# Kernel tuning notes

Measured on AMD Instinct MI355X. Metric: run time of the kernel, lower is better.

The kernel has to match this reference:

```python
import jax, jax.numpy as jnp
import numpy as np

B, N, K = 2, 128, 32   # batch, num_agents, irrep embedding dim
KAPPA = 1.0            # kappa_beta temperature
EPS = 1e-8             # cholesky regularization
EPS_SOFT = 1e-8        # softmax stability constant


def setup_inputs() -> dict:
    key = jax.random.key(0)
    k1, k2, k3, k4 = jax.random.split(key, 4)
    mu_q = jax.random.normal(k1, (B, N, K), jnp.float32)
    A = jax.random.normal(k2, (B, N, K, K), jnp.float32)
    # SPD belief covariances: A A^T / K + I
    sigma_q = jnp.einsum('bnkl,bnml->bnkm', A, A) / K + jnp.eye(K, dtype=jnp.float32)
    phi = 0.1 * jax.random.normal(k3, (B, N, 3), jnp.float32)  # small gauge frames
    G = jax.random.normal(k4, (3, K, K), jnp.float32)
    generators = 0.5 * (G - jnp.swapaxes(G, -1, -2))  # antisymmetric so(3) generators
    return {"mu_q": mu_q, "sigma_q": sigma_q, "phi": phi, "generators": generators}


def _expm_batched(X):
    # batched Pade matrix exponential over leading dims
    shp = X.shape
    Y = jax.vmap(jax.scipy.linalg.expm)(X.reshape(-1, shp[-2], shp[-1]))
    return Y.reshape(shp)


def reference(mu_q, sigma_q, phi, generators):
    Bb, Nn, Kk = mu_q.shape
    eye = jnp.eye(Kk, dtype=mu_q.dtype)

    # per-agent gauge frame exponentials: E_n = exp(phi_n . G), Em_n = exp(-phi_n . G)
    X = jnp.einsum('bna,akl->bnkl', phi, generators)
    E = _expm_batched(X)        # (B,N,K,K)
    Em = _expm_batched(-X)      # (B,N,K,K)

    # transported means: Omega_ij mu_j = E_i (Em_j mu_j)
    v = jnp.einsum('bjkl,bjl->bjk', Em, mu_q)              # (B,N,K)
    mu_t = jnp.einsum('bikl,bjl->bijk', E, v)              # (B,N,N,K)

    # transported covariances: Omega_ij Sigma_j Omega_ij^T = E_i (Em_j Sig_j Em_j^T) E_i^T
    S = jnp.einsum('bjkl,bjlm,bjnm->bjkn', Em, sigma_q, Em)          # (B,N,K,K)
    sig_t = jnp.einsum('bikl,bjlm,binm->bijkn', E, S, E)             # (B,N,N,K,K)
    sig_t = 0.5 * (sig_t + jnp.swapaxes(sig_t, -1, -2))              # symmetrize

    # KL(q_i || Omega_ij[q_j]) via Cholesky + triangular solves
    L1 = jnp.linalg.cholesky(sigma_q + EPS * eye)                    # (B,N,K,K)
    L2 = jnp.linalg.cholesky(sig_t + EPS * eye)                      # (B,N,N,K,K)

    # tr(Sig2^{-1} Sig1) = ||L2^{-1} L1||_F^2
    L1b = jnp.broadcast_to(L1[:, :, None], L2.shape)
    Aij = jax.scipy.linalg.solve_triangular(L2, L1b, lower=True)
    trace_term = jnp.sum(Aij * Aij, axis=(-2, -1))                   # (B,N,N)

    # (mu2-mu1)^T Sig2^{-1} (mu2-mu1) = ||L2^{-1} dmu||^2
    dmu = mu_t - mu_q[:, :, None, :]
    y = jax.scipy.linalg.solve_triangular(L2, dmu[..., None], lower=True)[..., 0]
    quad_term = jnp.sum(y * y, axis=-1)                              # (B,N,N)

    logdet1 = 2.0 * jnp.sum(jnp.log(jnp.diagonal(L1, axis1=-2, axis2=-1)), axis=-1)  # (B,N)
    logdet2 = 2.0 * jnp.sum(jnp.log(jnp.diagonal(L2, axis1=-2, axis2=-1)), axis=-1)  # (B,N,N)

    kl = 0.5 * (trace_term + quad_term - Kk + logdet2 - logdet1[:, :, None])
    kl = jnp.maximum(kl, 0.0)

    # attention weights beta_ij = softmax_j(-KL/kappa), then epsilon-renormalize
    beta = jax.nn.softmax(-kl / KAPPA, axis=-1)
    beta = beta + EPS_SOFT
    beta = beta / jnp.sum(beta, axis=-1, keepdims=True)

    # mean-only aggregation: m_i = sum_j beta_ij Omega_ij[mu_j]
    mu_agg = jnp.einsum('bij,bijk->bik', beta, mu_t)
    return mu_agg
```

## Files before the change

kernel.cpp:

```cpp
#include <hip/hip_runtime.h>
#include <math.h>

#define NB 2
#define NA 128
#define KD 32
#define LS 36
#define BN (NB*NA)
#define EPSV 1e-8f

__device__ __align__(16) float g_Q[BN*KD*KD];
__device__ __align__(16) float g_T[BN*KD*KD];
__device__ __align__(16) float g_E[BN*KD*KD];
__device__ __align__(16) float g_v[BN*KD];
__device__ __align__(16) float g_u[BN*KD];
__device__ __align__(16) float g_ld[BN];
__device__ __align__(16) float g_c[BN];

#define O_M   0
#define O_X   1152
#define O_X2  2304
#define O_X4  3456
#define O_B   4608
#define O_W   5760
#define O_E   6912
#define O_F   8064
#define O_VV  9216
#define O_DG  9248
#define O_P   9280
#define O_MU  9792
#define O_LD  9824
#define O_TOT 9828

__device__ __forceinline__ float rdlane(float x, int l) {
  return __int_as_float(__builtin_amdgcn_readlane(__float_as_int(x), l));
}
__device__ __forceinline__ float d4(float4 a, float4 b) {
  return a.x*b.x + a.y*b.y + a.z*b.z + a.w*b.w;
}

__device__ __forceinline__ void mm2(const float* A, const float* B,
                                    int r0, int c0, float acc[2]) {
  #pragma unroll
  for (int q4 = 0; q4 < KD; q4 += 4) {
    const float4 a4 = *(const float4*)&A[r0*LS + q4];
    const float ar[4] = {a4.x, a4.y, a4.z, a4.w};
    #pragma unroll
    for (int u = 0; u < 4; ++u) {
      const float2 b2 = *(const float2*)&B[(q4+u)*LS + c0];
      acc[0] += ar[u]*b2.x; acc[1] += ar[u]*b2.y;
    }
  }
}

__global__ __launch_bounds__(512, 1) void agent_kernel(
    const float* __restrict__ mu_q, const float* __restrict__ sigma_q,
    const float* __restrict__ phi, const float* __restrict__ gen) {
  __shared__ __align__(16) float buf[O_TOT];
  const int g = blockIdx.x;
  const int tid = threadIdx.x;
  const int e0 = tid * 2;
  const int r0 = e0 >> 5;
  const int c0 = e0 & 31;

  const float p0 = phi[g*3+0], p1 = phi[g*3+1], p2 = phi[g*3+2];
  if (tid < KD) buf[O_MU + tid] = mu_q[g*KD + tid];
  {
    const float2 sg = *(const float2*)(sigma_q + (size_t)g*1024 + e0);
    const float2 g0 = *(const float2*)(gen + e0);
    const float2 g1 = *(const float2*)(gen + 1024 + e0);
    const float2 g2 = *(const float2*)(gen + 2048 + e0);
    buf[O_X + r0*LS + c0]     = p0*g0.x + p1*g1.x + p2*g2.x;
    buf[O_X + r0*LS + c0 + 1] = p0*g0.y + p1*g1.y + p2*g2.y;
    buf[O_M + r0*LS + c0]     = sg.x + ((r0 == c0)     ? EPSV : 0.f);
    buf[O_M + r0*LS + c0 + 1] = sg.y + ((r0 == c0 + 1) ? EPSV : 0.f);
  }
  __syncthreads();

  float a2[2] = {0.f, 0.f};
  mm2(buf + O_X, buf + O_X, r0, c0, a2);
  if (c0 == r0)          buf[O_DG + r0] = a2[0];
  else if (c0 + 1 == r0) buf[O_DG + r0] = a2[1];
  __syncthreads();

  float trc = 0.f;
  #pragma unroll
  for (int r = 0; r < KD; ++r) trc += buf[O_DG + r];
  const float anorm = sqrtf(fmaxf(-trc, 0.f));
  int s = 0;
  if (anorm > 1.f) { s = (int)ceilf(log2f(anorm)); s = min(s, 15); }
  const float sc1 = exp2f((float)(-s));
  const float sc2 = sc1 * sc1;
  const float x2v0 = a2[0]*sc2, x2v1 = a2[1]*sc2;
  buf[O_X2 + r0*LS + c0]     = x2v0;
  buf[O_X2 + r0*LS + c0 + 1] = x2v1;
  __syncthreads();

  const float C4 = 1.f/24.f, C5 = 1.f/120.f, C6 = 1.f/720.f, C7 = 1.f/5040.f;
  float a3[2] = {0.f,0.f}, a4[2] = {0.f,0.f};
  mm2(buf + O_X2, buf + O_X,  r0, c0, a3);
  mm2(buf + O_X2, buf + O_X2, r0, c0, a4);
  const float dlt0 = (r0 == c0) ? 1.f : 0.f, dlt1 = (r0 == c0+1) ? 1.f : 0.f;
  const float xs0 = buf[O_X + r0*LS + c0]*sc1, xs1 = buf[O_X + r0*LS + c0+1]*sc1;
  const float x3v0 = a3[0]*sc1, x3v1 = a3[1]*sc1;
  buf[O_X4 + r0*LS + c0]     = a4[0];
  buf[O_X4 + r0*LS + c0 + 1] = a4[1];
  buf[O_B + r0*LS + c0]      = C4*dlt0 + C5*xs0 + C6*x2v0 + C7*x3v0;
  buf[O_B + r0*LS + c0 + 1]  = C4*dlt1 + C5*xs1 + C6*x2v1 + C7*x3v1;
  __syncthreads();

  {
    float u[2] = {0.f, 0.f};
    mm2(buf + O_B, buf + O_X4, r0, c0, u);
    buf[O_E + r0*LS + c0]     = dlt0 + xs0 + 0.5f*x2v0 + (1.f/6.f)*x3v0 + u[0];
    buf[O_E + r0*LS + c0 + 1] = dlt1 + xs1 + 0.5f*x2v1 + (1.f/6.f)*x3v1 + u[1];
  }
  __syncthreads();

  float* pe = buf + O_E;
  float* po = buf + O_F;
  for (int t = 0; t < s; ++t) {
    float ac[2] = {0.f, 0.f};
    mm2(pe, pe, r0, c0, ac);
    po[r0*LS + c0]     = ac[0];
    po[r0*LS + c0 + 1] = ac[1];
    __syncthreads();
    float* tp = pe; pe = po; po = tp;
  }

  if (tid < 64) {
    const int ci = tid & 31;
    float acc[KD];
    #pragma unroll
    for (int r = 0; r < KD; ++r) acc[r] = pe[r*LS + ci];
    float row[KD];
    #pragma unroll
    for (int q4 = 0; q4 < KD; q4 += 4) {
      const float4 m4 = *(const float4*)&buf[O_M + ci*LS + q4];
      row[q4] = m4.x; row[q4+1] = m4.y; row[q4+2] = m4.z; row[q4+3] = m4.w;
    }
    float Lr[KD], dinv[KD];
    float dprod = 1.f;
    #pragma unroll
    for (int j = 0; j < KD; ++j) {
      const float djj = rdlane(row[j], j);
      const float d = sqrtf(djj);
      const float rin = 1.f / d;
      dprod *= d;
      dinv[j] = rin;
      const float lij = row[j] * rin;
      Lr[j] = lij;
      #pragma unroll
      for (int q = j + 1; q < KD; ++q)
        row[q] = fmaf(-lij, rdlane(lij, q), row[q]);
    }
    if (tid == 0) {
      const float ld = 2.f * logf(dprod);
      g_ld[g] = ld;
      buf[O_LD] = ld;
    }
    #pragma unroll
    for (int q = 0; q < KD; ++q) {
      const float wq = acc[q] * dinv[q];
      acc[q] = wq;
      #pragma unroll
      for (int r = q + 1; r < KD; ++r)
        acc[r] = fmaf(-rdlane(Lr[q], r), wq, acc[r]);
    }
    #pragma unroll
    for (int r = 0; r < KD; ++r) buf[O_W + r*LS + ci] = acc[r];
  } else if (tid < 96) {
    const int c = tid - 64;
    float va = 0.f;
    #pragma unroll
    for (int r = 0; r < KD; ++r) va += pe[r*LS + c] * buf[O_MU + r];
    g_v[g*KD + c] = va;
    buf[O_VV + c] = va;
  } else if (tid >= 256) {
    const int t4 = (tid - 256) * 4;
    const int rm = t4 >> 5, cm = t4 & 31;
    float a[4] = {0.f,0.f,0.f,0.f};
    #pragma unroll
    for (int q4 = 0; q4 < KD; q4 += 4) {
      const float4 a4 = *(const float4*)&buf[O_M + rm*LS + q4];
      const float ar[4] = {a4.x, a4.y, a4.z, a4.w};
      #pragma unroll
      for (int u = 0; u < 4; ++u) {
        const float4 b4 = *(const float4*)&pe[(q4+u)*LS + cm];
        a[0] += ar[u]*b4.x; a[1] += ar[u]*b4.y;
        a[2] += ar[u]*b4.z; a[3] += ar[u]*b4.w;
      }
    }
    #pragma unroll
    for (int m = 0; m < 4; ++m) buf[O_B + rm*LS + cm + m] = a[m];
  }
  __syncthreads();

  {
    float aq[2] = {0.f,0.f}, at[2] = {0.f,0.f};
    #pragma unroll
    for (int q = 0; q < KD; ++q) {
      const float wq = buf[O_W + q*LS + r0];
      const float eq = pe[q*LS + r0];
      const float2 wb = *(const float2*)&buf[O_W + q*LS + c0];
      const float2 mb = *(const float2*)&buf[O_B + q*LS + c0];
      aq[0] += wq*wb.x; aq[1] += wq*wb.y;
      at[0] += eq*mb.x; at[1] += eq*mb.y;
    }
    const float vr = buf[O_VV + r0];
    const float vc0 = buf[O_VV + c0], vc1 = buf[O_VV + c0 + 1];
    at[0] += vr * vc0;
    at[1] += vr * vc1;
    *(float2*)&g_Q[(size_t)g*1024 + r0*KD + c0] = make_float2(aq[0], aq[1]);
    *(float2*)&g_T[(size_t)g*1024 + r0*KD + c0] = make_float2(at[0], at[1]);
    *(float2*)&g_E[(size_t)g*1024 + r0*KD + c0] =
        make_float2(pe[r0*LS + c0], pe[r0*LS + c0 + 1]);
    buf[O_P + r0*16 + (c0 >> 1)] = aq[0]*vc0 + aq[1]*vc1;
  }
  __syncthreads();

  if (tid < KD) {
    float u = 0.f;
    #pragma unroll
    for (int m = 0; m < 16; ++m) u += buf[O_P + tid*16 + m];
    g_u[g*KD + tid] = u;
    float t = u * buf[O_VV + tid];
    #pragma unroll
    for (int o = 1; o < 32; o <<= 1) t += __shfl_xor(t, o);
    if (tid == 0) g_c[g] = 0.5f*(t + buf[O_LD] - (float)KD);
  }
}

__global__ __launch_bounds__(512, 1) void pair_kernel(float* __restrict__ out) {
  const int g = blockIdx.x;
  const int b = g >> 7;
  const int i = g & (NA - 1);
  const int tid = threadIdx.x;
  __shared__ __align__(16) float sv[NA*KD];
  __shared__ __align__(16) float su[NA*KD];
  __shared__ float sc[NA];
  __shared__ float skl[NA];
  __shared__ float sbe[NA];
  __shared__ float sp[16*KD];
  __shared__ float sw[KD];

  {
    const float4* vs = (const float4*)(g_v + (size_t)b*NA*KD);
    const float4* us = (const float4*)(g_u + (size_t)b*NA*KD);
    float4* dv = (float4*)sv;
    float4* du = (float4*)su;
    dv[tid]       = vs[tid];
    dv[tid + 512] = vs[tid + 512];
    du[tid]       = us[tid];
    du[tid + 512] = us[tid + 512];
    if (tid < NA) sc[tid] = g_c[b*NA + tid];
  }

  const int lane = tid & 63;
  const int wave = tid >> 6;
  const int k  = lane >> 1;
  const int l0 = (lane & 1) * 16;
  const bool even = (lane & 1) == 0;

  float4 t0, t1, t2, t3;
  {
    const float4* Tp = (const float4*)(g_T + (size_t)g*1024 + k*KD + l0);
    t0 = Tp[0]; t1 = Tp[1]; t2 = Tp[2]; t3 = Tp[3];
  }
  const float ldi = g_ld[g];
  __syncthreads();

  const float vik = sv[i*KD + k];
  const float* Qb = g_Q + (size_t)b*NA*1024 + k*KD + l0;

  #pragma unroll 2
  for (int j = wave; j < NA; j += 8) {
    const float4* Qp = (const float4*)(Qb + (size_t)j*1024);
    const float4 q0 = Qp[0], q1 = Qp[1], q2 = Qp[2], q3 = Qp[3];
    float part = 0.5f*(d4(q0,t0) + d4(q1,t1) + d4(q2,t2) + d4(q3,t3));
    if (even) part = fmaf(-su[j*KD + k], vik, part);
    #pragma unroll
    for (int o = 1; o < 64; o <<= 1) part += __shfl_xor(part, o);
    if (lane == 0)
      skl[j] = fmaxf(part + sc[j] - 0.5f*ldi, 0.f);
  }
  __syncthreads();

  if (tid < 64) {
    const float a = skl[tid], c = skl[tid + 64];
    float mn = fminf(a, c);
    #pragma unroll
    for (int o = 1; o < 64; o <<= 1) mn = fminf(mn, __shfl_xor(mn, o));
    const float ea = expf(mn - a);
    const float eb = expf(mn - c);
    float sm = ea + eb;
    #pragma unroll
    for (int o = 1; o < 64; o <<= 1) sm += __shfl_xor(sm, o);
    const float inv = 1.f / sm;
    const float ren = 1.0f / (1.0f + 128.0f * 1e-8f);
    sbe[tid]      = (ea*inv + 1e-8f) * ren;
    sbe[tid + 64] = (eb*inv + 1e-8f) * ren;
  }
  __syncthreads();

  {
    const int c = tid >> 5, kk = tid & 31;
    float acc = 0.f;
    #pragma unroll
    for (int jj = 0; jj < 8; ++jj) {
      const int j = c*8 + jj;
      acc += sbe[j] * sv[j*KD + kk];
    }
    sp[c*KD + kk] = acc;
  }
  __syncthreads();
  if (tid < KD) {
    float w = 0.f;
    #pragma unroll
    for (int c2 = 0; c2 < 16; ++c2) w += sp[c2*KD + tid];
    sw[tid] = w;
  }
  __syncthreads();
  if (tid < KD) {
    const float* Ei = g_E + (size_t)g*1024 + tid*KD;
    float acc = 0.f;
    #pragma unroll
    for (int l = 0; l < KD; ++l) acc += Ei[l] * sw[l];
    out[g*KD + tid] = acc;
  }
}

extern "C" void kernel_launch(void* const* d_in, const int* in_sizes, int n_in,
                              void* d_out, int out_size, void* d_ws, size_t ws_size,
                              hipStream_t stream) {
  (void)in_sizes; (void)n_in; (void)out_size; (void)d_ws; (void)ws_size;
  const float* mu_q    = (const float*)d_in[0];
  const float* sigma_q = (const float*)d_in[1];
  const float* phi     = (const float*)d_in[2];
  const float* gen     = (const float*)d_in[3];
  float* out = (float*)d_out;
  hipLaunchKernelGGL(agent_kernel, dim3(BN), dim3(512), 0, stream,
                     mu_q, sigma_q, phi, gen);
  hipLaunchKernelGGL(pair_kernel, dim3(BN), dim3(512), 0, stream, out);
}
```

Before: 91.45 us.

## Use Frobenius norm for expm scaling and rework Cholesky via shared L

The scaling factor for the matrix exponential now comes from a wavefront-shuffle reduction of the Frobenius norm of X, not from the trace of X^2 computed by a full matmul. The X^2 product then runs unscaled and the powers are rescaled afterwards, which removes one matmul phase and one barrier ahead of the norm. The Cholesky factor is written to shared memory (reusing the X region) by a single wavefront of 32 threads instead of 64. Forward substitution then reads L from shared memory rather than broadcasting it with readlane. Template recursion forces full unrolling; the shared-memory reads in the substitution may cost more than the register broadcasts they replace.

```diff
diff --git a/kernel.cpp b/kernel.cpp
--- a/kernel.cpp
+++ b/kernel.cpp
@@ -30,6 +30,7 @@
 #define O_MU  9792
 #define O_LD  9824
 #define O_TOT 9828
+#define O_L   O_X
 
 __device__ __forceinline__ float rdlane(float x, int l) {
   return __int_as_float(__builtin_amdgcn_readlane(__float_as_int(x), l));
@@ -51,6 +52,44 @@
     }
   }
 }
+
+template<int J> struct Chol {
+  static __device__ __forceinline__ void run(float (&row)[KD], float (&dinv)[KD],
+                                             float& dprod, float* sL, int ci) {
+    const float djj = rdlane(row[J], J);
+    const float d = sqrtf(djj);
+    const float rin = 1.f / d;
+    dprod *= d;
+    dinv[J] = rin;
+    const float lij = row[J] * rin;
+    sL[ci*LS + J] = lij;
+    #pragma unroll
+    for (int q = J + 1; q < KD; ++q)
+      row[q] = fmaf(-lij, rdlane(lij, q), row[q]);
+    Chol<J+1>::run(row, dinv, dprod, sL, ci);
+  }
+};
+template<> struct Chol<KD> {
+  static __device__ __forceinline__ void run(float (&)[KD], float (&)[KD],
+                                             float&, float*, int) {}
+};
+
+template<int Q> struct Subst {
+  static __device__ __forceinline__ void run(float (&acc)[KD],
+                                             const float (&dinv)[KD],
+                                             const float* sL) {
+    const float wq = acc[Q] * dinv[Q];
+    acc[Q] = wq;
+    #pragma unroll
+    for (int r = Q + 1; r < KD; ++r)
+      acc[r] = fmaf(-sL[r*LS + Q], wq, acc[r]);
+    Subst<Q+1>::run(acc, dinv, sL);
+  }
+};
+template<> struct Subst<KD> {
+  static __device__ __forceinline__ void run(float (&)[KD], const float (&)[KD],
+                                             const float*) {}
+};
 
 __global__ __launch_bounds__(512, 1) void agent_kernel(
     const float* __restrict__ mu_q, const float* __restrict__ sigma_q,
@@ -64,55 +103,68 @@
 
   const float p0 = phi[g*3+0], p1 = phi[g*3+1], p2 = phi[g*3+2];
   if (tid < KD) buf[O_MU + tid] = mu_q[g*KD + tid];
+  float x0, x1;
   {
     const float2 sg = *(const float2*)(sigma_q + (size_t)g*1024 + e0);
     const float2 g0 = *(const float2*)(gen + e0);
     const float2 g1 = *(const float2*)(gen + 1024 + e0);
     const float2 g2 = *(const float2*)(gen + 2048 + e0);
-    buf[O_X + r0*LS + c0]     = p0*g0.x + p1*g1.x + p2*g2.x;
-    buf[O_X + r0*LS + c0 + 1] = p0*g0.y + p1*g1.y + p2*g2.y;
+    x0 = p0*g0.x + p1*g1.x + p2*g2.x;
+    x1 = p0*g0.y + p1*g1.y + p2*g2.y;
+    buf[O_X + r0*LS + c0]     = x0;
+    buf[O_X + r0*LS + c0 + 1] = x1;
     buf[O_M + r0*LS + c0]     = sg.x + ((r0 == c0)     ? EPSV : 0.f);
     buf[O_M + r0*LS + c0 + 1] = sg.y + ((r0 == c0 + 1) ? EPSV : 0.f);
   }
-  __syncthreads();
-
-  float a2[2] = {0.f, 0.f};
-  mm2(buf + O_X, buf + O_X, r0, c0, a2);
-  if (c0 == r0)          buf[O_DG + r0] = a2[0];
-  else if (c0 + 1 == r0) buf[O_DG + r0] = a2[1];
-  __syncthreads();
-
-  float trc = 0.f;
+  {
+    float nrm = x0*x0 + x1*x1;
+    #pragma unroll
+    for (int o = 1; o < 64; o <<= 1) nrm += __shfl_xor(nrm, o);
+    if ((tid & 63) == 0) buf[O_DG + (tid >> 6)] = nrm;
+  }
+  __syncthreads();
+
+  float snrm = 0.f;
   #pragma unroll
-  for (int r = 0; r < KD; ++r) trc += buf[O_DG + r];
-  const float anorm = sqrtf(fmaxf(-trc, 0.f));
+  for (int w = 0; w < 8; ++w) snrm += buf[O_DG + w];
+  const float anorm = sqrtf(snrm);
   int s = 0;
   if (anorm > 1.f) { s = (int)ceilf(log2f(anorm)); s = min(s, 15); }
   const float sc1 = exp2f((float)(-s));
-  const float sc2 = sc1 * sc1;
-  const float x2v0 = a2[0]*sc2, x2v1 = a2[1]*sc2;
-  buf[O_X2 + r0*LS + c0]     = x2v0;
-  buf[O_X2 + r0*LS + c0 + 1] = x2v1;
+  const float sc2 = sc1*sc1, sc3 = sc2*sc1, sc4 = sc2*sc2;
+
+  {
+    float a2[2] = {0.f, 0.f};
+    mm2(buf + O_X, buf + O_X, r0, c0, a2);
+    buf[O_X2 + r0*LS + c0]     = a2[0];
+    buf[O_X2 + r0*LS + c0 + 1] = a2[1];
+  }
   __syncthreads();
 
   const float C4 = 1.f/24.f, C5 = 1.f/120.f, C6 = 1.f/720.f, C7 = 1.f/5040.f;
-  float a3[2] = {0.f,0.f}, a4[2] = {0.f,0.f};
-  mm2(buf + O_X2, buf + O_X,  r0, c0, a3);
-  mm2(buf + O_X2, buf + O_X2, r0, c0, a4);
+  float x3v0, x3v1;
   const float dlt0 = (r0 == c0) ? 1.f : 0.f, dlt1 = (r0 == c0+1) ? 1.f : 0.f;
-  const float xs0 = buf[O_X + r0*LS + c0]*sc1, xs1 = buf[O_X + r0*LS + c0+1]*sc1;
-  const float x3v0 = a3[0]*sc1, x3v1 = a3[1]*sc1;
-  buf[O_X4 + r0*LS + c0]     = a4[0];
-  buf[O_X4 + r0*LS + c0 + 1] = a4[1];
-  buf[O_B + r0*LS + c0]      = C4*dlt0 + C5*xs0 + C6*x2v0 + C7*x3v0;
-  buf[O_B + r0*LS + c0 + 1]  = C4*dlt1 + C5*xs1 + C6*x2v1 + C7*x3v1;
+  {
+    float a3[2] = {0.f,0.f}, a4[2] = {0.f,0.f};
+    mm2(buf + O_X2, buf + O_X,  r0, c0, a3);
+    mm2(buf + O_X2, buf + O_X2, r0, c0, a4);
+    const float xs0 = buf[O_X + r0*LS + c0]*sc1, xs1 = buf[O_X + r0*LS + c0+1]*sc1;
+    const float x2s0 = buf[O_X2 + r0*LS + c0]*sc2, x2s1 = buf[O_X2 + r0*LS + c0+1]*sc2;
+    x3v0 = a3[0]*sc3; x3v1 = a3[1]*sc3;
+    buf[O_X4 + r0*LS + c0]     = a4[0]*sc4;
+    buf[O_X4 + r0*LS + c0 + 1] = a4[1]*sc4;
+    buf[O_B + r0*LS + c0]      = C4*dlt0 + C5*xs0 + C6*x2s0 + C7*x3v0;
+    buf[O_B + r0*LS + c0 + 1]  = C4*dlt1 + C5*xs1 + C6*x2s1 + C7*x3v1;
+  }
   __syncthreads();
 
   {
     float u[2] = {0.f, 0.f};
     mm2(buf + O_B, buf + O_X4, r0, c0, u);
-    buf[O_E + r0*LS + c0]     = dlt0 + xs0 + 0.5f*x2v0 + (1.f/6.f)*x3v0 + u[0];
-    buf[O_E + r0*LS + c0 + 1] = dlt1 + xs1 + 0.5f*x2v1 + (1.f/6.f)*x3v1 + u[1];
+    const float xs0 = buf[O_X + r0*LS + c0]*sc1, xs1 = buf[O_X + r0*LS + c0+1]*sc1;
+    const float x2s0 = buf[O_X2 + r0*LS + c0]*sc2, x2s1 = buf[O_X2 + r0*LS + c0+1]*sc2;
+    buf[O_E + r0*LS + c0]     = dlt0 + xs0 + 0.5f*x2s0 + (1.f/6.f)*x3v0 + u[0];
+    buf[O_E + r0*LS + c0 + 1] = dlt1 + xs1 + 0.5f*x2s1 + (1.f/6.f)*x3v1 + u[1];
   }
   __syncthreads();
 
@@ -127,48 +179,29 @@
     float* tp = pe; pe = po; po = tp;
   }
 
-  if (tid < 64) {
-    const int ci = tid & 31;
-    float acc[KD];
-    #pragma unroll
-    for (int r = 0; r < KD; ++r) acc[r] = pe[r*LS + ci];
+  if (tid < 32) {
+    const int ci = tid;
     float row[KD];
     #pragma unroll
     for (int q4 = 0; q4 < KD; q4 += 4) {
       const float4 m4 = *(const float4*)&buf[O_M + ci*LS + q4];
       row[q4] = m4.x; row[q4+1] = m4.y; row[q4+2] = m4.z; row[q4+3] = m4.w;
     }
-    float Lr[KD], dinv[KD];
+    float dinv[KD];
     float dprod = 1.f;
-    #pragma unroll
-    for (int j = 0; j < KD; ++j) {
-      const float djj = rdlane(row[j], j);
-      const float d = sqrtf(djj);
-      const float rin = 1.f / d;
-      dprod *= d;
-      dinv[j] = rin;
-      const float lij = row[j] * rin;
-      Lr[j] = lij;
-      #pragma unroll
-      for (int q = j + 1; q < KD; ++q)
-        row[q] = fmaf(-lij, rdlane(lij, q), row[q]);
-    }
+    Chol<0>::run(row, dinv, dprod, buf + O_L, ci);
     if (tid == 0) {
       const float ld = 2.f * logf(dprod);
       g_ld[g] = ld;
       buf[O_LD] = ld;
     }
-    #pragma unroll
-    for (int q = 0; q < KD; ++q) {
-      const float wq = acc[q] * dinv[q];
-      acc[q] = wq;
-      #pragma unroll
-      for (int r = q + 1; r < KD; ++r)
-        acc[r] = fmaf(-rdlane(Lr[q], r), wq, acc[r]);
-    }
+    float acc[KD];
+    #pragma unroll
+    for (int r = 0; r < KD; ++r) acc[r] = pe[r*LS + ci];
+    Subst<0>::run(acc, dinv, buf + O_L);
     #pragma unroll
     for (int r = 0; r < KD; ++r) buf[O_W + r*LS + ci] = acc[r];
-  } else if (tid < 96) {
+  } else if (tid >= 64 && tid < 96) {
     const int c = tid - 64;
     float va = 0.f;
     #pragma unroll
```

Result: no change. 90.85 us (-0.7%).
